# Performance work log

Measured on AMD Instinct MI355X. Metric: run time of the kernel, lower is better.

Reference implementation:

```python
import jax, jax.numpy as jnp
import numpy as np

B, C, T, D = 4, 64, 256, 256   # batch, channel, time, in_feat
H, DK, OUT = 4, 64, 256        # heads, d_k, out_feat
MIN_VALUE = float(np.finfo(np.float32).min)


def _complex_linear(xr, xi, wr, wi, br, bi):
    # ComplexLinear: (fc_r(xr) - fc_i(xi), fc_r(xi) + fc_i(xr))
    out_r = (xr @ wr + br) - (xi @ wi + bi)
    out_i = (xi @ wr + br) + (xr @ wi + bi)
    return out_r, out_i


def setup_inputs() -> dict:
    key = jax.random.key(0)
    ks = jax.random.split(key, 23)
    s = 1.0 / np.sqrt(D)
    inp = {}
    names = ['q_r', 'q_i', 'k_r', 'k_i', 'v_r', 'v_i']
    for i, n in enumerate(names):
        inp[n] = jax.random.normal(ks[i], (B, C, T, D), dtype=jnp.float32)
    inp['mask'] = jnp.ones((B, 1, C), dtype=jnp.int32)
    pi = 6
    for proj in ['q', 'k', 'v', 'o']:
        out_dim = OUT if proj == 'o' else D
        inp[f'w{proj}_r'] = jax.random.normal(ks[pi], (D, out_dim), dtype=jnp.float32) * s; pi += 1
        inp[f'w{proj}_i'] = jax.random.normal(ks[pi], (D, out_dim), dtype=jnp.float32) * s; pi += 1
        inp[f'b{proj}_r'] = jax.random.normal(ks[pi], (out_dim,), dtype=jnp.float32) * 0.01; pi += 1
        inp[f'b{proj}_i'] = jax.random.normal(ks[pi], (out_dim,), dtype=jnp.float32) * 0.01; pi += 1
    return inp


def _split_heads(x):
    # (B, C, T, D) -> (B, H, T, C, DK)  [view + transpose(1,3)]
    return x.reshape(B, C, T, H, DK).transpose(0, 3, 2, 1, 4)


def _attention(q_r, q_i, k_r, k_i, v_r, v_i, mask,
               wq_r, wq_i, bq_r, bq_i, wk_r, wk_i, bk_r, bk_i,
               wv_r, wv_i, bv_r, bv_i, wo_r, wo_i, bo_r, bo_i):
    qr, qi = _complex_linear(q_r, q_i, wq_r, wq_i, bq_r, bq_i)
    kr, ki = _complex_linear(k_r, k_i, wk_r, wk_i, bk_r, bk_i)
    vr, vi = _complex_linear(v_r, v_i, wv_r, wv_i, bv_r, bv_i)
    qr, qi, kr, ki, vr, vi = map(_split_heads, (qr, qi, kr, ki, vr, vi))

    # scores = conj(q) @ k^T  (conjugate_transpose_matmul_conjugate), scaled by 1/sqrt(d_k)
    scale = 1.0 / np.sqrt(DK)
    s_r = (jnp.einsum('bhtcd,bhted->bhtce', qr, kr)
           + jnp.einsum('bhtcd,bhted->bhtce', qi, ki)) * scale
    s_i = (jnp.einsum('bhtcd,bhted->bhtce', qr, ki)
           - jnp.einsum('bhtcd,bhted->bhtce', qi, kr)) * scale

    # amplitude softmax with masking (mask: (B,1,C) -> (B,1,1,1,C), eq(0))
    mask_b = (mask == 0)[:, None, None]  # (B,1,1,1,C)
    amp = jnp.sqrt(s_r * s_r + s_i * s_i)
    amp = jnp.where(mask_b, MIN_VALUE, amp)
    sc = jax.nn.softmax(amp, axis=-1) / amp
    a_r = jnp.where(mask_b, 0.0, sc * s_r)
    a_i = jnp.where(mask_b, 0.0, sc * s_i)

    # complex matmul attn @ v
    x_r = (jnp.einsum('bhtce,bhted->bhtcd', a_r, vr)
           - jnp.einsum('bhtce,bhted->bhtcd', a_i, vi))
    x_i = (jnp.einsum('bhtce,bhted->bhtcd', a_i, vr)
           + jnp.einsum('bhtce,bhted->bhtcd', a_r, vi))

    # (B,H,T,C,DK) -> (B,C,T,H*DK)
    x_r = x_r.transpose(0, 3, 2, 1, 4).reshape(B, C, T, H * DK)
    x_i = x_i.transpose(0, 3, 2, 1, 4).reshape(B, C, T, H * DK)
    return _complex_linear(x_r, x_i, wo_r, wo_i, bo_r, bo_i)


def reference(q_r, q_i, k_r, k_i, v_r, v_i, mask,
              wq_r, wq_i, bq_r, bq_i, wk_r, wk_i, bk_r, bk_i,
              wv_r, wv_i, bv_r, bv_i, wo_r, wo_i, bo_r, bo_i):
    return _attention(q_r, q_i, k_r, k_i, v_r, v_i, mask,
                      wq_r, wq_i, bq_r, bq_i, wk_r, wk_i, bk_r, bk_i,
                      wv_r, wv_i, bv_r, bv_i, wo_r, wo_i, bo_r, bo_i)
```

## Files before the change

kernel.cpp:

```cpp
#include <hip/hip_runtime.h>
#include <hip/hip_bf16.h>
#include <cstddef>

#define MIN_VALUE_F (-3.402823466e38f)


typedef __attribute__((ext_vector_type(8))) __bf16 bfrag;
typedef __attribute__((ext_vector_type(4))) float f32x4;

__device__ __forceinline__ float bf2f(unsigned int u) {
    union { unsigned int i; float f; } v; v.i = u << 16; return v.f;
}
__device__ __forceinline__ unsigned short f2bf(float f) {
    union { float f; unsigned int i; } v; v.f = f;
    return (unsigned short)((v.i + 0x7fffu + ((v.i >> 16) & 1u)) >> 16);
}
__device__ __forceinline__ unsigned int cvt2(float a, float b) {
    __hip_bfloat16 lo = __float2bfloat16(a);
    __hip_bfloat16 hi = __float2bfloat16(b);
    union { __hip_bfloat16 h[2]; unsigned int u; } x;
    x.h[0] = lo; x.h[1] = hi;
    return x.u;
}
__device__ __forceinline__ bfrag negf(bfrag v) {
    union { bfrag b; unsigned int u[4]; } x; x.b = v;
    #pragma unroll
    for (int i = 0; i < 4; ++i) x.u[i] ^= 0x80008000u;
    return x.b;
}

typedef __attribute__((address_space(3))) void lds_void_t;
typedef const __attribute__((address_space(1))) void gmem_void_t;
__device__ __forceinline__ void glds16(const void* g, void* l) {
    __builtin_amdgcn_global_load_lds((gmem_void_t*)g, (lds_void_t*)l, 16, 0, 0);
}

__device__ __forceinline__ bfrag rdfrag(const unsigned short* arr, int row, int slot) {
    const int s = slot ^ (row & 7);
    return *(const bfrag*)&arr[row * 64 + s * 8];
}

__global__ __launch_bounds__(256)
void wprep_kernel(const float* __restrict__ w0, const float* __restrict__ w1,
                  const float* __restrict__ w2, const float* __restrict__ w3,
                  const float* __restrict__ w4, const float* __restrict__ w5,
                  unsigned short* __restrict__ dst)
{
    const int my = blockIdx.y;
    const float* wsrc[6] = {w0, w1, w2, w3, w4, w5};
    const float* w = wsrc[my];
    const int cid = blockIdx.x * 256 + threadIdx.x;
    const int ss = cid & 3;
    const int n  = (cid >> 2) & 63;
    const int s  = (cid >> 8) & 7;
    const int nt = (cid >> 11) & 3;
    const int nn = nt * 64 + n;
    const int kb = s * 32 + ((ss ^ ((n >> 1) & 3)) << 3);
    unsigned int p[4];
    #pragma unroll
    for (int jj = 0; jj < 4; ++jj) {
        const float a = w[(size_t)(kb + 2 * jj) * 256 + nn];
        const float b = w[(size_t)(kb + 2 * jj + 1) * 256 + nn];
        p[jj] = cvt2(a, b);
    }
    uint4 q; q.x = p[0]; q.y = p[1]; q.z = p[2]; q.w = p[3];
    *(uint4*)&dst[(size_t)my * 65536 + (size_t)cid * 8] = q;
}

__global__ __launch_bounds__(256, 4)
void proj_mfma(const float* __restrict__ xq_r, const float* __restrict__ xq_i,
               const float* __restrict__ xk_r, const float* __restrict__ xk_i,
               const float* __restrict__ xv_r, const float* __restrict__ xv_i,
               const unsigned short* __restrict__ wimg,
               const float* __restrict__ bq_r, const float* __restrict__ bq_i,
               const float* __restrict__ bk_r, const float* __restrict__ bk_i,
               const float* __restrict__ bv_r, const float* __restrict__ bv_i,
               unsigned short* __restrict__ ws_out)
{
    __shared__ __align__(16) unsigned short SH[16384];

    const int bid = blockIdx.x;
    const int work = (bid & 7) * 1536 + (bid >> 3);
    const int ny = work & 3;
    const int rest = work >> 2;
    const int m0 = (rest & 1023) * 64;
    const int pz = rest >> 10;

    const float *xr, *xi, *br_, *bi_;
    if (pz == 0)      { xr = xq_r; xi = xq_i; br_ = bq_r; bi_ = bq_i; }
    else if (pz == 1) { xr = xk_r; xi = xk_i; br_ = bk_r; bi_ = bk_i; }
    else              { xr = xv_r; xi = xv_i; br_ = bv_r; bi_ = bv_i; }
    unsigned short* outr = ws_out + (size_t)pz * 2 * 16777216;
    unsigned short* outi = outr + 16777216;

    const int tid = threadIdx.x;
    const int lane = tid & 63, wv = tid >> 6;
    const int l15 = lane & 15, hi = lane >> 4;
    const int wm = (wv >> 1) * 32, wn = (wv & 1) * 32;

    const unsigned short* wr_img = wimg + (size_t)pz * 131072 + ny * 16384;
    const unsigned short* wi_img = wr_img + 65536;

    const int arow = tid >> 2;
    const int apos = tid & 3;
    const int asw = apos ^ ((arow >> 1) & 3);
    const int aidx = arow * 32 + (asw << 3);
    float4 fr0, fr1, fi0, fi1;
    uint4 wbr, wbi;

    f32x4 accR[2][2] = {}, accI[2][2] = {};

    auto load_step = [&](int s) {
        const size_t o = (size_t)(m0 + arow) * 256 + s * 32 + apos * 8;
        fr0 = *(const float4*)(xr + o);
        fr1 = *(const float4*)(xr + o + 4);
        fi0 = *(const float4*)(xi + o);
        fi1 = *(const float4*)(xi + o + 4);
        wbr = *(const uint4*)(wr_img + s * 2048 + tid * 8);
        wbi = *(const uint4*)(wi_img + s * 2048 + tid * 8);
    };
    auto write_stage = [&](int buf) {
        unsigned short* B = SH + buf * 8192;
        uint4 p, q;
        p.x = cvt2(fr0.x, fr0.y); p.y = cvt2(fr0.z, fr0.w);
        p.z = cvt2(fr1.x, fr1.y); p.w = cvt2(fr1.z, fr1.w);
        q.x = cvt2(fi0.x, fi0.y); q.y = cvt2(fi0.z, fi0.w);
        q.z = cvt2(fi1.x, fi1.y); q.w = cvt2(fi1.z, fi1.w);
        *(uint4*)&B[aidx] = p;
        *(uint4*)&B[2048 + aidx] = q;
        *(uint4*)&B[4096 + tid * 8] = wbr;
        *(uint4*)&B[6144 + tid * 8] = wbi;
    };

    load_step(0);
    write_stage(0);
    __syncthreads();

    for (int s = 0; s < 8; ++s) {
        const int b = s & 1;
        if (s < 7) load_step(s + 1);
        const unsigned short* As_r = SH + b * 8192;
        const unsigned short* As_i = As_r + 2048;
        const unsigned short* Ws_r = As_r + 4096;
        const unsigned short* Ws_i = As_r + 6144;
        bfrag ar[2], ai[2], nai[2];
        #pragma unroll
        for (int mf = 0; mf < 2; ++mf) {
            const int m = wm + mf * 16 + l15;
            const int idx = m * 32 + ((hi ^ ((m >> 1) & 3)) << 3);
            ar[mf] = *(const bfrag*)&As_r[idx];
            ai[mf] = *(const bfrag*)&As_i[idx];
            nai[mf] = negf(ai[mf]);
        }
        #pragma unroll
        for (int nf = 0; nf < 2; ++nf) {
            const int n = wn + nf * 16 + l15;
            const int idx = n * 32 + ((hi ^ ((n >> 1) & 3)) << 3);
            const bfrag brf = *(const bfrag*)&Ws_r[idx];
            const bfrag bif = *(const bfrag*)&Ws_i[idx];
            #pragma unroll
            for (int mf = 0; mf < 2; ++mf) {
                accR[mf][nf] = __builtin_amdgcn_mfma_f32_16x16x32_bf16(ar[mf], brf, accR[mf][nf], 0, 0, 0);
                accR[mf][nf] = __builtin_amdgcn_mfma_f32_16x16x32_bf16(nai[mf], bif, accR[mf][nf], 0, 0, 0);
                accI[mf][nf] = __builtin_amdgcn_mfma_f32_16x16x32_bf16(ai[mf], brf, accI[mf][nf], 0, 0, 0);
                accI[mf][nf] = __builtin_amdgcn_mfma_f32_16x16x32_bf16(ar[mf], bif, accI[mf][nf], 0, 0, 0);
            }
        }
        if (s < 7) write_stage(b ^ 1);
        __syncthreads();
    }

    const int bc = m0 >> 8, b = bc >> 6, c = bc & 63, t0 = m0 & 255;
    #pragma unroll
    for (int nf = 0; nf < 2; ++nf) {
        const int n_loc = wn + nf * 16 + l15;
        const int n_glob = ny * 64 + n_loc;
        const float vbr = br_[n_glob], vbi = bi_[n_glob];
        const float addR = vbr - vbi, addI = vbr + vbi;
        #pragma unroll
        for (int mf = 0; mf < 2; ++mf) {
            #pragma unroll
            for (int r = 0; r < 4; ++r) {
                const int m_loc = wm + mf * 16 + hi * 4 + r;
                SH[m_loc * 64 + n_loc] = f2bf(accR[mf][nf][r] + addR);
                SH[4096 + m_loc * 64 + n_loc] = f2bf(accI[mf][nf][r] + addI);
            }
        }
    }
    __syncthreads();
    const int h = ny;
    #pragma unroll
    for (int p = 0; p < 2; ++p) {
        const int tr = (tid >> 3) + p * 32;
        const int dk = (tid & 7) * 8;
        const int L = tr * 64 + dk;
        const size_t g = (((size_t)(b * 4 + h) * 256 + (t0 + tr)) * 64 + c) * 64 + dk;
        *(uint4*)&outr[g] = *(const uint4*)&SH[L];
        *(uint4*)&outi[g] = *(const uint4*)&SH[4096 + L];
    }
}

__global__ __launch_bounds__(256)
void attn_mfma(const unsigned short* __restrict__ Qg_r, const unsigned short* __restrict__ Qg_i,
               const unsigned short* __restrict__ Kg_r, const unsigned short* __restrict__ Kg_i,
               const unsigned short* __restrict__ Vg_r, const unsigned short* __restrict__ Vg_i,
               const int* __restrict__ mask,
               unsigned short* __restrict__ Xr, unsigned short* __restrict__ Xi)
{
    __shared__ __align__(16) unsigned short sQr[4096], sQi[4096];
    __shared__ __align__(16) unsigned short sKr[4096], sKi[4096];
    __shared__ __align__(16) unsigned short sVr[4608], sVi[4608];
    __shared__ int smask[64];

    const int bht = blockIdx.x;
    const int b = bht >> 10;
    const int h = (bht >> 8) & 3;
    const int t = bht & 255;
    const size_t base = (size_t)bht * 4096;
    const int tid = threadIdx.x;
    const int lane = tid & 63, wv = tid >> 6;
    const int l15 = lane & 15, hi = lane >> 4;

    const int ep = (lane & 31) * 2;
    const int dch = wv * 2 + (lane >> 5);
    const unsigned short* vr0p = Vg_r + base + (size_t)ep * 64 + dch * 8;
    const unsigned short* vi0p = Vg_i + base + (size_t)ep * 64 + dch * 8;
    const uint4 vr0 = *(const uint4*)vr0p;
    const uint4 vr1 = *(const uint4*)(vr0p + 64);
    const uint4 vi0 = *(const uint4*)vi0p;
    const uint4 vi1 = *(const uint4*)(vi0p + 64);

    #pragma unroll
    for (int i = 0; i < 2; ++i) {
        const int ch = wv * 128 + i * 64 + lane;
        const int r = ch >> 3, cg = ch & 7;
        const int so = r * 64 + ((cg ^ (r & 7)) << 3);
        const int dofs = (wv * 128 + i * 64) << 3;
        glds16(Qg_r + base + so, &sQr[dofs]);
        glds16(Qg_i + base + so, &sQi[dofs]);
        glds16(Kg_r + base + so, &sKr[dofs]);
        glds16(Kg_i + base + so, &sKi[dofs]);
    }
    if (tid < 64) smask[tid] = mask[b * 64 + tid];

    {
        union { uint4 v; unsigned short s[8]; } ar0, ar1, ai0, ai1;
        ar0.v = vr0; ar1.v = vr1; ai0.v = vi0; ai1.v = vi1;
        #pragma unroll
        for (int j = 0; j < 8; ++j) {
            const int d = dch * 8 + j;
            *(unsigned int*)&sVr[d * 72 + ep] = (unsigned)ar0.s[j] | ((unsigned)ar1.s[j] << 16);
            *(unsigned int*)&sVi[d * 72 + ep] = (unsigned)ai0.s[j] | ((unsigned)ai1.s[j] << 16);
        }
    }
    __syncthreads();

    const int cq = wv * 16 + l15;
    f32x4 aR[4] = {}, aI[4] = {};
    #pragma unroll
    for (int ks = 0; ks < 2; ++ks) {
        const int slot = ks * 4 + hi;
        const bfrag qr = rdfrag(sQr, cq, slot);
        const bfrag qi = rdfrag(sQi, cq, slot);
        const bfrag nqi = negf(qi);
        #pragma unroll
        for (int et = 0; et < 4; ++et) {
            const int re = et * 16 + l15;
            const bfrag kr = rdfrag(sKr, re, slot);
            const bfrag ki = rdfrag(sKi, re, slot);
            aR[et] = __builtin_amdgcn_mfma_f32_16x16x32_bf16(kr, qr, aR[et], 0, 0, 0);
            aR[et] = __builtin_amdgcn_mfma_f32_16x16x32_bf16(ki, qi, aR[et], 0, 0, 0);
            aI[et] = __builtin_amdgcn_mfma_f32_16x16x32_bf16(ki, qr, aI[et], 0, 0, 0);
            aI[et] = __builtin_amdgcn_mfma_f32_16x16x32_bf16(kr, nqi, aI[et], 0, 0, 0);
        }
    }
    __syncthreads();

    const float scale = 0.125f;
    float amp[4][4], ex[4][4];
    float mx = MIN_VALUE_F;
    #pragma unroll
    for (int et = 0; et < 4; ++et) {
        #pragma unroll
        for (int r = 0; r < 4; ++r) {
            const float sr = aR[et][r] * scale;
            const float si = aI[et][r] * scale;
            float a = sqrtf(fmaf(sr, sr, si * si));
            if (smask[et * 16 + hi * 4 + r] == 0) a = MIN_VALUE_F;
            amp[et][r] = a;
            mx = fmaxf(mx, a);
        }
    }
    mx = fmaxf(mx, __shfl_xor(mx, 16, 64));
    mx = fmaxf(mx, __shfl_xor(mx, 32, 64));
    float sm = 0.f;
    #pragma unroll
    for (int et = 0; et < 4; ++et) {
        #pragma unroll
        for (int r = 0; r < 4; ++r) {
            const float e_ = expf(amp[et][r] - mx);
            ex[et][r] = e_; sm += e_;
        }
    }
    sm += __shfl_xor(sm, 16, 64);
    sm += __shfl_xor(sm, 32, 64);

    #pragma unroll
    for (int et = 0; et < 4; ++et) {
        float pr[4], pi[4];
        #pragma unroll
        for (int r = 0; r < 4; ++r) {
            const float w = ex[et][r] * __builtin_amdgcn_rcpf(sm * amp[et][r]);
            pr[r] = w * (aR[et][r] * scale);
            pi[r] = w * (aI[et][r] * scale);
        }
        const int pidx = cq * 64 + ((et * 16 + hi * 4) ^ ((cq & 7) << 3));
        uint2 ur, ui;
        ur.x = cvt2(pr[0], pr[1]); ur.y = cvt2(pr[2], pr[3]);
        ui.x = cvt2(pi[0], pi[1]); ui.y = cvt2(pi[2], pi[3]);
        *(uint2*)&sQr[pidx] = ur;
        *(uint2*)&sQi[pidx] = ui;
    }
    __syncthreads();

    f32x4 xR4[4] = {}, xI4[4] = {};
    #pragma unroll
    for (int ks = 0; ks < 2; ++ks) {
        const int slot = ks * 4 + hi;
        const bfrag pr = rdfrag(sQr, cq, slot);
        const bfrag pi = rdfrag(sQi, cq, slot);
        const bfrag npi = negf(pi);
        #pragma unroll
        for (int dt = 0; dt < 4; ++dt) {
            const int rd = dt * 16 + l15;
            const bfrag vr = *(const bfrag*)&sVr[rd * 72 + ks * 32 + hi * 8];
            const bfrag vi = *(const bfrag*)&sVi[rd * 72 + ks * 32 + hi * 8];
            xR4[dt] = __builtin_amdgcn_mfma_f32_16x16x32_bf16(pr, vr, xR4[dt], 0, 0, 0);
            xR4[dt] = __builtin_amdgcn_mfma_f32_16x16x32_bf16(npi, vi, xR4[dt], 0, 0, 0);
            xI4[dt] = __builtin_amdgcn_mfma_f32_16x16x32_bf16(pi, vr, xI4[dt], 0, 0, 0);
            xI4[dt] = __builtin_amdgcn_mfma_f32_16x16x32_bf16(pr, vi, xI4[dt], 0, 0, 0);
        }
    }

    #pragma unroll
    for (int dt = 0; dt < 4; ++dt) {
        #pragma unroll
        for (int r = 0; r < 4; ++r) {
            const int c = wv * 16 + hi * 4 + r;
            const size_t o = (((size_t)(b * 64 + c) * 256) + t) * 256 + h * 64 + dt * 16 + l15;
            Xr[o] = f2bf(xR4[dt][r]);
            Xi[o] = f2bf(xI4[dt][r]);
        }
    }
}

__global__ __launch_bounds__(256, 4)
void oproj_mfma(const unsigned short* __restrict__ Xr_g, const unsigned short* __restrict__ Xi_g,
                const unsigned short* __restrict__ wimg,
                const float* __restrict__ bo_r, const float* __restrict__ bo_i,
                float* __restrict__ outr, float* __restrict__ outi)
{
    __shared__ __align__(16) unsigned short SH[16384];

    const int bid = blockIdx.x;
    const int work = (bid & 7) * 512 + (bid >> 3);
    const int ny = work & 3;
    const int m0 = (work >> 2) * 64;

    const int tid = threadIdx.x;
    const int lane = tid & 63, wv = tid >> 6;
    const int l15 = lane & 15, hi = lane >> 4;
    const int wm = (wv >> 1) * 32, wn = (wv & 1) * 32;

    const unsigned short* wr_img = wimg + ny * 16384;
    const unsigned short* wi_img = wr_img + 65536;

    const int xrow = tid >> 2;
    const int xslot = tid & 3;
    const int xsw = xslot ^ ((xrow >> 1) & 3);
    const int xidx = xrow * 32 + xslot * 8;
    uint4 xbr, xbi, wbr, wbi;

    f32x4 accR[2][2] = {}, accI[2][2] = {};

    auto load_step = [&](int s) {
        const size_t o = (size_t)(m0 + xrow) * 256 + s * 32 + xsw * 8;
        xbr = *(const uint4*)(Xr_g + o);
        xbi = *(const uint4*)(Xi_g + o);
        wbr = *(const uint4*)(wr_img + s * 2048 + tid * 8);
        wbi = *(const uint4*)(wi_img + s * 2048 + tid * 8);
    };
    auto write_stage = [&](int buf) {
        unsigned short* B = SH + buf * 8192;
        *(uint4*)&B[xidx] = xbr;
        *(uint4*)&B[2048 + xidx] = xbi;
        *(uint4*)&B[4096 + tid * 8] = wbr;
        *(uint4*)&B[6144 + tid * 8] = wbi;
    };

    load_step(0);
    write_stage(0);
    __syncthreads();

    for (int s = 0; s < 8; ++s) {
        const int b = s & 1;
        if (s < 7) load_step(s + 1);
        const unsigned short* As_r = SH + b * 8192;
        const unsigned short* As_i = As_r + 2048;
        const unsigned short* Ws_r = As_r + 4096;
        const unsigned short* Ws_i = As_r + 6144;
        bfrag ar[2], ai[2], nai[2];
        #pragma unroll
        for (int mf = 0; mf < 2; ++mf) {
            const int m = wm + mf * 16 + l15;
            const int idx = m * 32 + ((hi ^ ((m >> 1) & 3)) << 3);
            ar[mf] = *(const bfrag*)&As_r[idx];
            ai[mf] = *(const bfrag*)&As_i[idx];
            nai[mf] = negf(ai[mf]);
        }
        #pragma unroll
        for (int nf = 0; nf < 2; ++nf) {
            const int n = wn + nf * 16 + l15;
            const int idx = n * 32 + ((hi ^ ((n >> 1) & 3)) << 3);
            const bfrag brf = *(const bfrag*)&Ws_r[idx];
            const bfrag bif = *(const bfrag*)&Ws_i[idx];
            #pragma unroll
            for (int mf = 0; mf < 2; ++mf) {
                accR[mf][nf] = __builtin_amdgcn_mfma_f32_16x16x32_bf16(ar[mf], brf, accR[mf][nf], 0, 0, 0);
                accR[mf][nf] = __builtin_amdgcn_mfma_f32_16x16x32_bf16(nai[mf], bif, accR[mf][nf], 0, 0, 0);
                accI[mf][nf] = __builtin_amdgcn_mfma_f32_16x16x32_bf16(ai[mf], brf, accI[mf][nf], 0, 0, 0);
                accI[mf][nf] = __builtin_amdgcn_mfma_f32_16x16x32_bf16(ar[mf], bif, accI[mf][nf], 0, 0, 0);
            }
        }
        if (s < 7) write_stage(b ^ 1);
        __syncthreads();
    }

    #pragma unroll
    for (int nf = 0; nf < 2; ++nf) {
        const int n = ny * 64 + wn + nf * 16 + l15;
        const float vbr = bo_r[n], vbi = bo_i[n];
        const float addR = vbr - vbi, addI = vbr + vbi;
        #pragma unroll
        for (int mf = 0; mf < 2; ++mf) {
            #pragma unroll
            for (int r = 0; r < 4; ++r) {
                const size_t o = (size_t)(m0 + wm + mf * 16 + hi * 4 + r) * 256 + n;
                outr[o] = accR[mf][nf][r] + addR;
                outi[o] = accI[mf][nf][r] + addI;
            }
        }
    }
}

extern "C" void kernel_launch(void* const* d_in, const int* in_sizes, int n_in,
                              void* d_out, int out_size, void* d_ws, size_t ws_size,
                              hipStream_t stream)
{
    (void)in_sizes; (void)n_in; (void)out_size; (void)ws_size;
    const float* q_r = (const float*)d_in[0];
    const float* q_i = (const float*)d_in[1];
    const float* k_r = (const float*)d_in[2];
    const float* k_i = (const float*)d_in[3];
    const float* v_r = (const float*)d_in[4];
    const float* v_i = (const float*)d_in[5];
    const int* mask = (const int*)d_in[6];
    const float* wq_r = (const float*)d_in[7];
    const float* wq_i = (const float*)d_in[8];
    const float* bq_r = (const float*)d_in[9];
    const float* bq_i = (const float*)d_in[10];
    const float* wk_r = (const float*)d_in[11];
    const float* wk_i = (const float*)d_in[12];
    const float* bk_r = (const float*)d_in[13];
    const float* bk_i = (const float*)d_in[14];
    const float* wv_r = (const float*)d_in[15];
    const float* wv_i = (const float*)d_in[16];
    const float* bv_r = (const float*)d_in[17];
    const float* bv_i = (const float*)d_in[18];
    const float* wo_r = (const float*)d_in[19];
    const float* wo_i = (const float*)d_in[20];
    const float* bo_r = (const float*)d_in[21];
    const float* bo_i = (const float*)d_in[22];

    const size_t TS = 16777216;
    unsigned short* ws = (unsigned short*)d_ws;
    unsigned short* Q = ws;
    unsigned short* Xr = ws + 6 * TS;
    unsigned short* Xi = ws + 7 * TS;
    unsigned short* wimg_qkv = ws + 6 * TS;
    unsigned short* wimg_o = ws;

    wprep_kernel<<<dim3(32, 6), 256, 0, stream>>>(wq_r, wq_i, wk_r, wk_i, wv_r, wv_i, wimg_qkv);
    proj_mfma<<<dim3(12288), 256, 0, stream>>>(q_r, q_i, k_r, k_i, v_r, v_i, wimg_qkv,
                                               bq_r, bq_i, bk_r, bk_i, bv_r, bv_i, ws);
    attn_mfma<<<dim3(4096), 256, 0, stream>>>(Q, Q + TS, Q + 2 * TS, Q + 3 * TS,
                                              Q + 4 * TS, Q + 5 * TS, mask, Xr, Xi);
    wprep_kernel<<<dim3(32, 2), 256, 0, stream>>>(wo_r, wo_i, wo_r, wo_r, wo_r, wo_r, wimg_o);
    oproj_mfma<<<dim3(4096), 256, 0, stream>>>(Xr, Xi, wimg_o, bo_r, bo_i,
                                               (float*)d_out, (float*)d_out + TS);
}
```

Measured before the change: 332.2 us.

## Read weight fragments directly from global memory, precompute negated imaginary weights

The projection GEMM kernels no longer stage weight tiles through LDS. Each lane loads its MFMA B fragments straight from a pre-laid-out bf16 weight image that now also holds a negated copy of the imaginary weights, which removes the per-step negation. LDS per block is halved and launch bounds are raised to allow more resident blocks, which is meant to cut LDS traffic and raise occupancy. The cost is more global and L2 traffic for weight fragments that are not shared within a block, plus extra weight-prep launches.

```diff
diff --git a/kernel.cpp b/kernel.cpp
--- a/kernel.cpp
+++ b/kernel.cpp
@@ -41,33 +41,49 @@
 }
 
 __global__ __launch_bounds__(256)
-void wprep_kernel(const float* __restrict__ w0, const float* __restrict__ w1,
-                  const float* __restrict__ w2, const float* __restrict__ w3,
-                  const float* __restrict__ w4, const float* __restrict__ w5,
+void wprep_kernel(const float* __restrict__ wr, const float* __restrict__ wi,
                   unsigned short* __restrict__ dst)
 {
-    const int my = blockIdx.y;
-    const float* wsrc[6] = {w0, w1, w2, w3, w4, w5};
-    const float* w = wsrc[my];
+    const int which = blockIdx.y;
+    const float* w = (which == 0) ? wr : wi;
+    const float sgn = (which == 2) ? -1.f : 1.f;
     const int cid = blockIdx.x * 256 + threadIdx.x;
-    const int ss = cid & 3;
-    const int n  = (cid >> 2) & 63;
-    const int s  = (cid >> 8) & 7;
-    const int nt = (cid >> 11) & 3;
-    const int nn = nt * 64 + n;
-    const int kb = s * 32 + ((ss ^ ((n >> 1) & 3)) << 3);
+    const int u0 = cid * 8;
+    const int k  = u0 & 31;
+    const int n  = (u0 >> 5) & 63;
+    const int s  = (u0 >> 11) & 7;
+    const int nt = u0 >> 14;
+    const int col = nt * 64 + n;
+    const int kb = s * 32 + k;
     unsigned int p[4];
     #pragma unroll
     for (int jj = 0; jj < 4; ++jj) {
-        const float a = w[(size_t)(kb + 2 * jj) * 256 + nn];
-        const float b = w[(size_t)(kb + 2 * jj + 1) * 256 + nn];
+        const float a = sgn * w[(size_t)(kb + 2 * jj) * 256 + col];
+        const float b = sgn * w[(size_t)(kb + 2 * jj + 1) * 256 + col];
         p[jj] = cvt2(a, b);
     }
     uint4 q; q.x = p[0]; q.y = p[1]; q.z = p[2]; q.w = p[3];
-    *(uint4*)&dst[(size_t)my * 65536 + (size_t)cid * 8] = q;
-}
-
-__global__ __launch_bounds__(256, 4)
+    *(uint4*)&dst[(size_t)which * 65536 + u0] = q;
+}
+
+#define P_LOADA(s) { \
+    const size_t o_ = (size_t)(m0 + arow) * 256 + (s) * 32 + apos * 8; \
+    fr0 = *(const float4*)(xr + o_); \
+    fr1 = *(const float4*)(xr + o_ + 4); \
+    fi0 = *(const float4*)(xi + o_); \
+    fi1 = *(const float4*)(xi + o_ + 4); }
+
+#define P_WRITE(buf) { \
+    unsigned short* B_ = SH + (buf) * 4096; \
+    uint4 p_, q_; \
+    p_.x = cvt2(fr0.x, fr0.y); p_.y = cvt2(fr0.z, fr0.w); \
+    p_.z = cvt2(fr1.x, fr1.y); p_.w = cvt2(fr1.z, fr1.w); \
+    q_.x = cvt2(fi0.x, fi0.y); q_.y = cvt2(fi0.z, fi0.w); \
+    q_.z = cvt2(fi1.x, fi1.y); q_.w = cvt2(fi1.z, fi1.w); \
+    *(uint4*)&B_[aidx] = p_; \
+    *(uint4*)&B_[2048 + aidx] = q_; }
+
+__global__ __launch_bounds__(256, 5)
 void proj_mfma(const float* __restrict__ xq_r, const float* __restrict__ xq_i,
                const float* __restrict__ xk_r, const float* __restrict__ xk_i,
                const float* __restrict__ xv_r, const float* __restrict__ xv_i,
@@ -77,7 +93,7 @@
                const float* __restrict__ bv_r, const float* __restrict__ bv_i,
                unsigned short* __restrict__ ws_out)
 {
-    __shared__ __align__(16) unsigned short SH[16384];
+    __shared__ __align__(16) unsigned short SH[8192];
 
     const int bid = blockIdx.x;
     const int work = (bid & 7) * 1536 + (bid >> 3);
@@ -98,75 +114,56 @@
     const int l15 = lane & 15, hi = lane >> 4;
     const int wm = (wv >> 1) * 32, wn = (wv & 1) * 32;
 
-    const unsigned short* wr_img = wimg + (size_t)pz * 131072 + ny * 16384;
-    const unsigned short* wi_img = wr_img + 65536;
+    const unsigned short* wb = wimg + (size_t)pz * 196608 + ny * 16384;
+    const unsigned short* wr_img = wb;
+    const unsigned short* wi_img = wb + 65536;
+    const unsigned short* wn_img = wb + 131072;
 
     const int arow = tid >> 2;
     const int apos = tid & 3;
-    const int asw = apos ^ ((arow >> 1) & 3);
-    const int aidx = arow * 32 + (asw << 3);
+    const int aidx = arow * 32 + ((apos ^ ((arow >> 1) & 3)) << 3);
     float4 fr0, fr1, fi0, fi1;
-    uint4 wbr, wbi;
+
+    const int fb0 = (wn + l15) * 32 + hi * 8;
+    const int fb1 = (wn + 16 + l15) * 32 + hi * 8;
 
     f32x4 accR[2][2] = {}, accI[2][2] = {};
 
-    auto load_step = [&](int s) {
-        const size_t o = (size_t)(m0 + arow) * 256 + s * 32 + apos * 8;
-        fr0 = *(const float4*)(xr + o);
-        fr1 = *(const float4*)(xr + o + 4);
-        fi0 = *(const float4*)(xi + o);
-        fi1 = *(const float4*)(xi + o + 4);
-        wbr = *(const uint4*)(wr_img + s * 2048 + tid * 8);
-        wbi = *(const uint4*)(wi_img + s * 2048 + tid * 8);
-    };
-    auto write_stage = [&](int buf) {
-        unsigned short* B = SH + buf * 8192;
-        uint4 p, q;
-        p.x = cvt2(fr0.x, fr0.y); p.y = cvt2(fr0.z, fr0.w);
-        p.z = cvt2(fr1.x, fr1.y); p.w = cvt2(fr1.z, fr1.w);
-        q.x = cvt2(fi0.x, fi0.y); q.y = cvt2(fi0.z, fi0.w);
-        q.z = cvt2(fi1.x, fi1.y); q.w = cvt2(fi1.z, fi1.w);
-        *(uint4*)&B[aidx] = p;
-        *(uint4*)&B[2048 + aidx] = q;
-        *(uint4*)&B[4096 + tid * 8] = wbr;
-        *(uint4*)&B[6144 + tid * 8] = wbi;
-    };
-
-    load_step(0);
-    write_stage(0);
-    __syncthreads();
-
+    P_LOADA(0);
+    P_WRITE(0);
+    __syncthreads();
+
+    #pragma unroll
     for (int s = 0; s < 8; ++s) {
-        const int b = s & 1;
-        if (s < 7) load_step(s + 1);
-        const unsigned short* As_r = SH + b * 8192;
+        const bfrag br0 = *(const bfrag*)&wr_img[s * 2048 + fb0];
+        const bfrag br1 = *(const bfrag*)&wr_img[s * 2048 + fb1];
+        const bfrag bi0 = *(const bfrag*)&wi_img[s * 2048 + fb0];
+        const bfrag bi1 = *(const bfrag*)&wi_img[s * 2048 + fb1];
+        const bfrag nb0 = *(const bfrag*)&wn_img[s * 2048 + fb0];
+        const bfrag nb1 = *(const bfrag*)&wn_img[s * 2048 + fb1];
+        if (s < 7) P_LOADA(s + 1);
+        const unsigned short* As_r = SH + (s & 1) * 4096;
         const unsigned short* As_i = As_r + 2048;
-        const unsigned short* Ws_r = As_r + 4096;
-        const unsigned short* Ws_i = As_r + 6144;
-        bfrag ar[2], ai[2], nai[2];
+        bfrag ar[2], ai[2];
         #pragma unroll
         for (int mf = 0; mf < 2; ++mf) {
             const int m = wm + mf * 16 + l15;
             const int idx = m * 32 + ((hi ^ ((m >> 1) & 3)) << 3);
             ar[mf] = *(const bfrag*)&As_r[idx];
             ai[mf] = *(const bfrag*)&As_i[idx];
-            nai[mf] = negf(ai[mf]);
-        }
-        #pragma unroll
-        for (int nf = 0; nf < 2; ++nf) {
-            const int n = wn + nf * 16 + l15;
-            const int idx = n * 32 + ((hi ^ ((n >> 1) & 3)) << 3);
-            const bfrag brf = *(const bfrag*)&Ws_r[idx];
-            const bfrag bif = *(const bfrag*)&Ws_i[idx];
-            #pragma unroll
-            for (int mf = 0; mf < 2; ++mf) {
-                accR[mf][nf] = __builtin_amdgcn_mfma_f32_16x16x32_bf16(ar[mf], brf, accR[mf][nf], 0, 0, 0);
-                accR[mf][nf] = __builtin_amdgcn_mfma_f32_16x16x32_bf16(nai[mf], bif, accR[mf][nf], 0, 0, 0);
-                accI[mf][nf] = __builtin_amdgcn_mfma_f32_16x16x32_bf16(ai[mf], brf, accI[mf][nf], 0, 0, 0);
-                accI[mf][nf] = __builtin_amdgcn_mfma_f32_16x16x32_bf16(ar[mf], bif, accI[mf][nf], 0, 0, 0);
-            }
-        }
-        if (s < 7) write_stage(b ^ 1);
+        }
+        #pragma unroll
+        for (int mf = 0; mf < 2; ++mf) {
+            accR[mf][0] = __builtin_amdgcn_mfma_f32_16x16x32_bf16(ar[mf], br0, accR[mf][0], 0, 0, 0);
+            accR[mf][0] = __builtin_amdgcn_mfma_f32_16x16x32_bf16(ai[mf], nb0, accR[mf][0], 0, 0, 0);
+            accI[mf][0] = __builtin_amdgcn_mfma_f32_16x16x32_bf16(ai[mf], br0, accI[mf][0], 0, 0, 0);
+            accI[mf][0] = __builtin_amdgcn_mfma_f32_16x16x32_bf16(ar[mf], bi0, accI[mf][0], 0, 0, 0);
+            accR[mf][1] = __builtin_amdgcn_mfma_f32_16x16x32_bf16(ar[mf], br1, accR[mf][1], 0, 0, 0);
+            accR[mf][1] = __builtin_amdgcn_mfma_f32_16x16x32_bf16(ai[mf], nb1, accR[mf][1], 0, 0, 0);
+            accI[mf][1] = __builtin_amdgcn_mfma_f32_16x16x32_bf16(ai[mf], br1, accI[mf][1], 0, 0, 0);
+            accI[mf][1] = __builtin_amdgcn_mfma_f32_16x16x32_bf16(ar[mf], bi1, accI[mf][1], 0, 0, 0);
+        }
+        if (s < 7) P_WRITE((s + 1) & 1);
         __syncthreads();
     }
 
@@ -354,13 +351,23 @@
     }
 }
 
-__global__ __launch_bounds__(256, 4)
+#define O_LOADX(s) { \
+    const size_t o_ = (size_t)(m0 + xrow) * 256 + (s) * 32 + xsw * 8; \
+    xbr = *(const uint4*)(Xr_g + o_); \
+    xbi = *(const uint4*)(Xi_g + o_); }
+
+#define O_WRITE(buf) { \
+    unsigned short* B_ = SH + (buf) * 4096; \
+    *(uint4*)&B_[xidx] = xbr; \
+    *(uint4*)&B_[2048 + xidx] = xbi; }
+
+__global__ __launch_bounds__(256, 5)
 void oproj_mfma(const unsigned short* __restrict__ Xr_g, const unsigned short* __restrict__ Xi_g,
                 const unsigned short* __restrict__ wimg,
                 const float* __restrict__ bo_r, const float* __restrict__ bo_i,
                 float* __restrict__ outr, float* __restrict__ outi)
 {
-    __shared__ __align__(16) unsigned short SH[16384];
+    __shared__ __align__(16) unsigned short SH[8192];
 
     const int bid = blockIdx.x;
     const int work = (bid & 7) * 512 + (bid >> 3);
@@ -374,65 +381,54 @@
 
     const unsigned short* wr_img = wimg + ny * 16384;
     const unsigned short* wi_img = wr_img + 65536;
+    const unsigned short* wn_img = wr_img + 131072;
 
     const int xrow = tid >> 2;
-    const int xslot = tid & 3;
-    const int xsw = xslot ^ ((xrow >> 1) & 3);
-    const int xidx = xrow * 32 + xslot * 8;
-    uint4 xbr, xbi, wbr, wbi;
+    const int xpos = tid & 3;
+    const int xsw = xpos ^ ((xrow >> 1) & 3);
+    const int xidx = xrow * 32 + xpos * 8;
+    uint4 xbr, xbi;
+
+    const int fb0 = (wn + l15) * 32 + hi * 8;
+    const int fb1 = (wn + 16 + l15) * 32 + hi * 8;
 
     f32x4 accR[2][2] = {}, accI[2][2] = {};
 
-    auto load_step = [&](int s) {
-        const size_t o = (size_t)(m0 + xrow) * 256 + s * 32 + xsw * 8;
-        xbr = *(const uint4*)(Xr_g + o);
-        xbi = *(const uint4*)(Xi_g + o);
-        wbr = *(const uint4*)(wr_img + s * 2048 + tid * 8);
-        wbi = *(const uint4*)(wi_img + s * 2048 + tid * 8);
-    };
-    auto write_stage = [&](int buf) {
-        unsigned short* B = SH + buf * 8192;
-        *(uint4*)&B[xidx] = xbr;
-        *(uint4*)&B[2048 + xidx] = xbi;
-        *(uint4*)&B[4096 + tid * 8] = wbr;
-        *(uint4*)&B[6144 + tid * 8] = wbi;
-    };
-
-    load_step(0);
-    write_stage(0);
-    __syncthreads();
-
+    O_LOADX(0);
+    O_WRITE(0);
+    __syncthreads();
+
+    #pragma unroll
     for (int s = 0; s < 8; ++s) {
-        const int b = s & 1;
-        if (s < 7) load_step(s + 1);
-        const unsigned short* As_r = SH + b * 8192;
+        const bfrag br0 = *(const bfrag*)&wr_img[s * 2048 + fb0];
+        const bfrag br1 = *(const bfrag*)&wr_img[s * 2048 + fb1];
+        const bfrag bi0 = *(const bfrag*)&wi_img[s * 2048 + fb0];
+        const bfrag bi1 = *(const bfrag*)&wi_img[s * 2048 + fb1];
+        const bfrag nb0 = *(const bfrag*)&wn_img[s * 2048 + fb0];
+        const bfrag nb1 = *(const bfrag*)&wn_img[s * 2048 + fb1];
+        if (s < 7) O_LOADX(s + 1);
+        const unsigned short* As_r = SH + (s & 1) * 4096;
         const unsigned short* As_i = As_r + 2048;
-        const unsigned short* Ws_r = As_r + 4096;
-        const unsigned short* Ws_i = As_r + 6144;
-        bfrag ar[2], ai[2], nai[2];
+        bfrag ar[2], ai[2];
         #pragma unroll
         for (int mf = 0; mf < 2; ++mf) {
             const int m = wm + mf * 16 + l15;
             const int idx = m * 32 + ((hi ^ ((m >> 1) & 3)) << 3);
             ar[mf] = *(const bfrag*)&As_r[idx];
             ai[mf] = *(const bfrag*)&As_i[idx];
-            nai[mf] = negf(ai[mf]);
-        }
-        #pragma unroll
-        for (int nf = 0; nf < 2; ++nf) {
-            const int n = wn + nf * 16 + l15;
-            const int idx = n * 32 + ((hi ^ ((n >> 1) & 3)) << 3);
-            const bfrag brf = *(const bfrag*)&Ws_r[idx];
-            const bfrag bif = *(const bfrag*)&Ws_i[idx];
-            #pragma unroll
-            for (int mf = 0; mf < 2; ++mf) {
-                accR[mf][nf] = __builtin_amdgcn_mfma_f32_16x16x32_bf16(ar[mf], brf, accR[mf][nf], 0, 0, 0);
-                accR[mf][nf] = __builtin_amdgcn_mfma_f32_16x16x32_bf16(nai[mf], bif, accR[mf][nf], 0, 0, 0);
-                accI[mf][nf] = __builtin_amdgcn_mfma_f32_16x16x32_bf16(ai[mf], brf, accI[mf][nf], 0, 0, 0);
-                accI[mf][nf] = __builtin_amdgcn_mfma_f32_16x16x32_bf16(ar[mf], bif, accI[mf][nf], 0, 0, 0);
-            }
-        }
-        if (s < 7) write_stage(b ^ 1);
+        }
+        #pragma unroll
+        for (int mf = 0; mf < 2; ++mf) {
+            accR[mf][0] = __builtin_amdgcn_mfma_f32_16x16x32_bf16(ar[mf], br0, accR[mf][0], 0, 0, 0);
+            accR[mf][0] = __builtin_amdgcn_mfma_f32_16x16x32_bf16(ai[mf], nb0, accR[mf][0], 0, 0, 0);
+            accI[mf][0] = __builtin_amdgcn_mfma_f32_16x16x32_bf16(ai[mf], br0, accI[mf][0], 0, 0, 0);
+            accI[mf][0] = __builtin_amdgcn_mfma_f32_16x16x32_bf16(ar[mf], bi0, accI[mf][0], 0, 0, 0);
+            accR[mf][1] = __builtin_amdgcn_mfma_f32_16x16x32_bf16(ar[mf], br1, accR[mf][1], 0, 0, 0);
+            accR[mf][1] = __builtin_amdgcn_mfma_f32_16x16x32_bf16(ai[mf], nb1, accR[mf][1], 0, 0, 0);
+            accI[mf][1] = __builtin_amdgcn_mfma_f32_16x16x32_bf16(ai[mf], br1, accI[mf][1], 0, 0, 0);
+            accI[mf][1] = __builtin_amdgcn_mfma_f32_16x16x32_bf16(ar[mf], bi1, accI[mf][1], 0, 0, 0);
+        }
+        if (s < 7) O_WRITE((s + 1) & 1);
         __syncthreads();
     }
 
@@ -490,12 +486,14 @@
     unsigned short* wimg_qkv = ws + 6 * TS;
     unsigned short* wimg_o = ws;
 
-    wprep_kernel<<<dim3(32, 6), 256, 0, stream>>>(wq_r, wq_i, wk_r, wk_i, wv_r, wv_i, wimg_qkv);
+    wprep_kernel<<<dim3(32, 3), 256, 0, stream>>>(wq_r, wq_i, wimg_qkv);
+    wprep_kernel<<<dim3(32, 3), 256, 0, stream>>>(wk_r, wk_i, wimg_qkv + 196608);
+    wprep_kernel<<<dim3(32, 3), 256, 0, stream>>>(wv_r, wv_i, wimg_qkv + 393216);
     proj_mfma<<<dim3(12288), 256, 0, stream>>>(q_r, q_i, k_r, k_i, v_r, v_i, wimg_qkv,
                                                bq_r, bq_i, bk_r, bk_i, bv_r, bv_i, ws);
     attn_mfma<<<dim3(4096), 256, 0, stream>>>(Q, Q + TS, Q + 2 * TS, Q + 3 * TS,
                                               Q + 4 * TS, Q + 5 * TS, mask, Xr, Xi);
-    wprep_kernel<<<dim3(32, 2), 256, 0, stream>>>(wo_r, wo_i, wo_r, wo_r, wo_r, wo_r, wimg_o);
+    wprep_kernel<<<dim3(32, 3), 256, 0, stream>>>(wo_r, wo_i, wimg_o);
     oproj_mfma<<<dim3(4096), 256, 0, stream>>>(Xr, Xi, wimg_o, bo_r, bo_i,
                                                (float*)d_out, (float*)d_out + TS);
 }
```

New measurement: 415.5 us. 25.1% more time.
